# Performance work log

Hardware: AMD Instinct MI355X
Metric: run time of the kernel (lower is better)

The kernel has to match this reference:

```python
import jax, jax.numpy as jnp
import numpy as np

N_NODES = 20000
N_EDGES = 50000
IN_DIM = 128
HID = 128
OUT_DIM = 64
N_PAIRS = 128
N_LAYERS = 2
N_HEADS = 4


def setup_inputs() -> dict:
    key = jax.random.key(0)
    ks = jax.random.split(key, 32)
    s = 0.05
    def p(k, shape):
        return jax.random.normal(k, shape, jnp.float32) * s
    inp = {}
    inp["node_features"] = jax.random.normal(ks[0], (N_NODES, IN_DIM), jnp.float32)
    inp["edge_index"] = jax.random.randint(ks[1], (2, N_EDGES), 0, N_NODES, jnp.int32)
    inp["edge_timestamps"] = jax.random.uniform(ks[2], (N_EDGES,), jnp.float32)
    inp["target_pairs"] = jax.random.randint(ks[3], (N_PAIRS, 2), 0, N_NODES, jnp.int32)
    inp["in_W"] = p(ks[4], (HID, IN_DIM)); inp["in_b"] = p(ks[5], (HID,))
    inp["te_W1"] = p(ks[6], (N_LAYERS, HID, 1)); inp["te_b1"] = p(ks[7], (N_LAYERS, HID))
    inp["te_W2"] = p(ks[8], (N_LAYERS, HID, HID)); inp["te_b2"] = p(ks[9], (N_LAYERS, HID))
    inp["attn_in_W"] = p(ks[10], (N_LAYERS, 3 * HID, HID)); inp["attn_in_b"] = p(ks[11], (N_LAYERS, 3 * HID))
    inp["attn_out_W"] = p(ks[12], (N_LAYERS, HID, HID)); inp["attn_out_b"] = p(ks[13], (N_LAYERS, HID))
    inp["ft_W"] = p(ks[14], (N_LAYERS, HID, HID)); inp["ft_b"] = p(ks[15], (N_LAYERS, HID))
    inp["op_W"] = p(ks[16], (N_LAYERS, HID, HID)); inp["op_b"] = p(ks[17], (N_LAYERS, HID))
    inp["out1_W"] = p(ks[18], (HID, HID)); inp["out1_b"] = p(ks[19], (HID,))
    inp["out2_W"] = p(ks[20], (OUT_DIM, HID)); inp["out2_b"] = p(ks[21], (OUT_DIM,))
    inp["lp1_W"] = p(ks[22], (HID, 2 * OUT_DIM)); inp["lp1_b"] = p(ks[23], (HID,))
    inp["lp2_W"] = p(ks[24], (HID // 2, HID)); inp["lp2_b"] = p(ks[25], (HID // 2,))
    inp["lp3_W"] = p(ks[26], (1, HID // 2)); inp["lp3_b"] = p(ks[27], (1,))
    return inp


def _forward(node_features, edge_index, edge_timestamps, target_pairs,
             in_W, in_b, te_W1, te_b1, te_W2, te_b2,
             attn_in_W, attn_in_b, attn_out_W, attn_out_b,
             ft_W, ft_b, op_W, op_b,
             out1_W, out1_b, out2_W, out2_b,
             lp1_W, lp1_b, lp2_W, lp2_b, lp3_W, lp3_b):
    N = node_features.shape[0]
    h = in_W.shape[0]
    H = N_HEADS
    d = h // H
    scale = 1.0 / np.sqrt(d).astype(np.float32)
    src, dst = edge_index[0], edge_index[1]
    # flattened target nodes; duplicates compute identical rows so dedup (torch.unique) is unneeded
    targets = target_pairs.reshape(-1)  # [U]
    U = targets.shape[0]
    E = src.shape[0]

    x = node_features @ in_W.T + in_b  # [N, h]
    for l in range(te_W1.shape[0]):
        tf = x @ ft_W[l].T + ft_b[l]                                           # [N, h]
        tfeat = jax.nn.relu(edge_timestamps[:, None] @ te_W1[l].T + te_b1[l])
        tfeat = tfeat @ te_W2[l].T + te_b2[l]                                  # [E, h]
        Wq, Wk, Wv = jnp.split(attn_in_W[l], 3, axis=0)
        bq, bk, bv = jnp.split(attn_in_b[l], 3)
        q = (tf[targets] @ Wq.T + bq).reshape(U, H, d)
        # keys/values are linear in (tf[nbr] + tfeat): split into node term A and edge term B
        Ak = (tf @ Wk.T).reshape(N, H, d)
        Bk = (tfeat @ Wk.T + bk).reshape(E, H, d)
        Av = (tf @ Wv.T).reshape(N, H, d)
        Bv = (tfeat @ Wv.T + bv).reshape(E, H, d)
        is_src = src[None, :] == targets[:, None]          # [U, E]
        mask = is_src | (dst[None, :] == targets[:, None])  # edge incident to target
        nbr = jnp.where(is_src, dst[None, :], src[None, :])  # other endpoint, [U, E]
        qAk = jnp.einsum('uhd,nhd->uhn', q, Ak) * scale      # [U, H, N]
        idx = jnp.broadcast_to(nbr[:, None, :], (U, H, E))
        s_node = jnp.take_along_axis(qAk, idx, axis=2)        # [U, H, E]
        s_edge = jnp.einsum('uhd,ehd->uhe', q, Bk) * scale
        scores = jnp.where(mask[:, None, :], s_node + s_edge, -1e30)
        p = jax.nn.softmax(scores, axis=-1)
        p = jnp.where(mask[:, None, :], p, 0.0)               # [U, H, E]
        out_edge = jnp.einsum('uhe,ehd->uhd', p, Bv)
        # sum_e p * Av[nbr] via per-target scatter of probs into node space
        w = jax.vmap(lambda pe, ne: jax.ops.segment_sum(pe, ne, num_segments=N))(
            p.transpose(0, 2, 1), nbr)                        # [U, N, H]
        out_node = jnp.einsum('unh,nhd->uhd', w, Av)
        attn = (out_node + out_edge).reshape(U, h) @ attn_out_W[l].T + attn_out_b[l]
        has_nbr = mask.any(axis=1)
        agg_in = jnp.where(has_nbr[:, None], attn, tf[targets])
        agg = agg_in @ op_W[l].T + op_b[l]
        x = x.at[targets].set(agg)
        x = jax.nn.relu(x)
    emb = jax.nn.relu(x @ out1_W.T + out1_b) @ out2_W.T + out2_b  # [N, out]
    pair = jnp.concatenate([emb[target_pairs[:, 0]], emb[target_pairs[:, 1]]], axis=1)
    z = jax.nn.relu(pair @ lp1_W.T + lp1_b)
    z = jax.nn.relu(z @ lp2_W.T + lp2_b)
    return jax.nn.sigmoid(z @ lp3_W.T + lp3_b)  # [B, 1]


def reference(node_features, edge_index, edge_timestamps, target_pairs,
              in_W, in_b, te_W1, te_b1, te_W2, te_b2,
              attn_in_W, attn_in_b, attn_out_W, attn_out_b,
              ft_W, ft_b, op_W, op_b,
              out1_W, out1_b, out2_W, out2_b,
              lp1_W, lp1_b, lp2_W, lp2_b, lp3_W, lp3_b):
    return _forward(node_features, edge_index, edge_timestamps, target_pairs,
                    in_W, in_b, te_W1, te_b1, te_W2, te_b2,
                    attn_in_W, attn_in_b, attn_out_W, attn_out_b,
                    ft_W, ft_b, op_W, op_b,
                    out1_W, out1_b, out2_W, out2_b,
                    lp1_W, lp1_b, lp2_W, lp2_b, lp3_W, lp3_b)
```

## Files before the change

kernel.cpp:

```cpp
#include <hip/hip_runtime.h>
#include <math.h>

#define N_NODES 20000
#define N_EDGES 50000
#define N_SLOTS 256
#define N_PAIRS 128
#define CAP 32
#define MSTRIDE 16384
#define NMAT 19
#define TFLAG (1 << 30)
#define HSZ 1024
#define NBLK 256
#define BATCH 16

__device__ __forceinline__ float4 relu4(float4 v) {
    return make_float4(fmaxf(v.x, 0.f), fmaxf(v.y, 0.f), fmaxf(v.z, 0.f), fmaxf(v.w, 0.f));
}
__device__ __forceinline__ float4 add4(float4 a, float4 b) {
    return make_float4(a.x + b.x, a.y + b.y, a.z + b.z, a.w + b.w);
}
__device__ __forceinline__ void fma4(float4& acc, const float4 w, const float s) {
    acc.x = fmaf(w.x, s, acc.x); acc.y = fmaf(w.y, s, acc.y);
    acc.z = fmaf(w.z, s, acc.z); acc.w = fmaf(w.w, s, acc.w);
}
#define F4Z make_float4(0.f, 0.f, 0.f, 0.f)

__device__ __forceinline__ void gbar(unsigned* cnt, unsigned target, bool wait) {
    __syncthreads();
    if (threadIdx.x == 0) {
        __builtin_amdgcn_fence(__ATOMIC_RELEASE, "agent");
        __hip_atomic_fetch_add(cnt, 1u, __ATOMIC_RELAXED, __HIP_MEMORY_SCOPE_AGENT);
        if (wait) {
            int it = 0;
            while (true) {
                unsigned v;
                if ((it++ & 7) != 7)
                    v = __hip_atomic_load(cnt, __ATOMIC_RELAXED,
                                          __HIP_MEMORY_SCOPE_SYSTEM);
                else
                    v = __hip_atomic_fetch_add(cnt, 0u, __ATOMIC_RELAXED,
                                               __HIP_MEMORY_SCOPE_AGENT);
                if (v >= target) break;
                __builtin_amdgcn_s_sleep(16);
            }
            __builtin_amdgcn_fence(__ATOMIC_ACQUIRE, "agent");
        }
    }
    __syncthreads();
}

__device__ __forceinline__ float4 mv_ks1_g8(const float* __restrict__ WT,
                                            const float* __restrict__ xv128,
                                            int g, int jj) {
    const float4* W4 = (const float4*)WT;
    const float4* x4 = (const float4*)xv128;
    float4 acc = F4Z;
#pragma unroll
    for (int kk4 = 0; kk4 < 4; ++kk4) {
        int k4 = g * 4 + kk4;
        float4 xv = x4[k4];
        fma4(acc, W4[(k4 * 4 + 0) * 32 + jj], xv.x);
        fma4(acc, W4[(k4 * 4 + 1) * 32 + jj], xv.y);
        fma4(acc, W4[(k4 * 4 + 2) * 32 + jj], xv.z);
        fma4(acc, W4[(k4 * 4 + 3) * 32 + jj], xv.w);
    }
    return acc;
}
__device__ __forceinline__ float4 mv_ks1_g8_64(const float* __restrict__ WT,
                                               const float* __restrict__ xv128,
                                               int g, int jj) {
    const float4* W4 = (const float4*)WT;
    const float4* x4 = (const float4*)xv128;
    int j16 = jj & 15;
    float4 acc = F4Z;
#pragma unroll
    for (int kk4 = 0; kk4 < 4; ++kk4) {
        int k4 = g * 4 + kk4;
        float4 xv = x4[k4];
        fma4(acc, W4[(k4 * 4 + 0) * 16 + j16], xv.x);
        fma4(acc, W4[(k4 * 4 + 1) * 16 + j16], xv.y);
        fma4(acc, W4[(k4 * 4 + 2) * 16 + j16], xv.z);
        fma4(acc, W4[(k4 * 4 + 3) * 16 + j16], xv.w);
    }
    return acc;
}
__device__ __forceinline__ float4 comb1_g8(const float4* pb, int jj) {
    float4 s = pb[jj];
#pragma unroll
    for (int gp = 1; gp < 8; ++gp) s = add4(s, pb[gp * 32 + jj]);
    return s;
}

__device__ __forceinline__ void mv16_g8(const float* __restrict__ WT,
                                        const float* __restrict__ xs,
                                        int g, int jj, float4* acc) {
    const float4* W4 = (const float4*)WT;
    const float4* x4 = (const float4*)xs;
#pragma unroll
    for (int kk4 = 0; kk4 < 4; ++kk4) {
        int k4 = g * 4 + kk4;
        float4 w0 = W4[(k4 * 4 + 0) * 32 + jj];
        float4 w1 = W4[(k4 * 4 + 1) * 32 + jj];
        float4 w2 = W4[(k4 * 4 + 2) * 32 + jj];
        float4 w3 = W4[(k4 * 4 + 3) * 32 + jj];
#pragma unroll
        for (int e = 0; e < 16; ++e) {
            float4 xv = x4[e * 32 + k4];
            fma4(acc[e], w0, xv.x); fma4(acc[e], w1, xv.y);
            fma4(acc[e], w2, xv.z); fma4(acc[e], w3, xv.w);
        }
    }
}
__device__ __forceinline__ float4 comb16_g8(const float4* pb, int it, int jj) {
    float4 s = pb[it * 32 + jj];
#pragma unroll
    for (int gp = 1; gp < 8; ++gp) s = add4(s, pb[(gp * 16 + it) * 32 + jj]);
    return s;
}

__device__ __forceinline__ float4 mv_ks1(const float* __restrict__ WT,
                                         const float* __restrict__ xv128,
                                         int g, int jj) {
    const float4* W4 = (const float4*)WT;
    const float4* x4 = (const float4*)xv128;
    float4 acc = F4Z;
#pragma unroll 2
    for (int kk4 = 0; kk4 < 8; ++kk4) {
        int k4 = g * 8 + kk4;
        float4 xv = x4[k4];
        fma4(acc, W4[(k4 * 4 + 0) * 32 + jj], xv.x);
        fma4(acc, W4[(k4 * 4 + 1) * 32 + jj], xv.y);
        fma4(acc, W4[(k4 * 4 + 2) * 32 + jj], xv.z);
        fma4(acc, W4[(k4 * 4 + 3) * 32 + jj], xv.w);
    }
    return acc;
}
__device__ __forceinline__ float4 mv_ks1_64(const float* __restrict__ WT,
                                            const float* __restrict__ xv128,
                                            int g, int jj) {
    const float4* W4 = (const float4*)WT;
    const float4* x4 = (const float4*)xv128;
    int j16 = jj & 15;
    float4 acc = F4Z;
#pragma unroll 2
    for (int kk4 = 0; kk4 < 8; ++kk4) {
        int k4 = g * 8 + kk4;
        float4 xv = x4[k4];
        fma4(acc, W4[(k4 * 4 + 0) * 16 + j16], xv.x);
        fma4(acc, W4[(k4 * 4 + 1) * 16 + j16], xv.y);
        fma4(acc, W4[(k4 * 4 + 2) * 16 + j16], xv.z);
        fma4(acc, W4[(k4 * 4 + 3) * 16 + j16], xv.w);
    }
    return acc;
}
__device__ __forceinline__ float4 comb1(const float4* pb, int jj) {
    return add4(add4(pb[jj], pb[32 + jj]), add4(pb[64 + jj], pb[96 + jj]));
}

__device__ __forceinline__ unsigned thash(int key) {
    return ((unsigned)key * 2654435761u) >> 22;
}
__device__ __forceinline__ bool hexists(const int* __restrict__ hkey, int key) {
    unsigned h = thash(key);
    while (true) {
        int k = hkey[h];
        if (k == -1) return false;
        if (k == key) return true;
        h = (h + 1) & (HSZ - 1);
    }
}
__device__ __forceinline__ void hemit_g(const int* __restrict__ hkey,
                                        const int* __restrict__ hval,
                                        int* __restrict__ gcnt,
                                        int2* __restrict__ lst,
                                        int key, int e, int nbrf) {
    unsigned h = thash(key);
    while (true) {
        int k = hkey[h];
        if (k == -1) return;
        if (k == key) {
            int s = hval[h];
            int pos = atomicAdd(&gcnt[s], 1);
            if (pos < CAP) lst[s * CAP + pos] = make_int2(e, nbrf);
        }
        h = (h + 1) & (HSZ - 1);
    }
}

struct Params {
    const float* nf; const int* ei; const float* ts; const int* tp;
    const float* inW; const float* inb;
    const float* teW1; const float* teb1; const float* teW2; const float* teb2;
    const float* aiW; const float* aib; const float* aoW; const float* aob;
    const float* ftW; const float* ftb; const float* opW; const float* opb;
    const float* o1W; const float* o1b; const float* o2W; const float* o2b;
    const float* l1W; const float* l1b; const float* l2W; const float* l2b;
    const float* l3W; const float* l3b;
    float* out; float* x; int* cnt; int2* lst; float* emb; float* WT;
    unsigned* bar;
};

__global__ __launch_bounds__(256, 1) void k_fused(Params P) {
    __shared__ __align__(16) float xu[128], x0u[128], tfv[128], qv[128], sv[128];
    __shared__ __align__(16) float xs[BATCH * 128], t1s[BATCH * 128];
    __shared__ __align__(16) float x0s[BATCH * 128];
    __shared__ __align__(16) float zs[CAP * 128];
    __shared__ __align__(16) float4 pb[8 * 16 * 32];
    __shared__ __align__(16) float qkh[4 * 128];
    __shared__ __align__(16) float zbl[4 * 128];
    __shared__ float scl[CAP * 4], ps[CAP * 4], sbk[4];
    __shared__ int nbr_s[BATCH], tf_s[BATCH];
    __shared__ float ts_s[BATCH];
    __shared__ __align__(16) float tile[32][129];
    __shared__ int hkey[HSZ], hval[HSZ];

    const int b = blockIdx.x, tid = threadIdx.x, g = tid >> 5, jj = tid & 31;

    if (b < 72) {
        int m, r0, rows;
        if (b < 68) { m = b >> 2; r0 = (b & 3) * 32; rows = 128; }
        else { int mm = b - 68; m = 17 + (mm >> 1); r0 = (mm & 1) * 32; rows = 64; }
        const float* src;
        if (m == 0) src = P.inW;
        else if (m <= 2) src = P.ftW + (m - 1) * MSTRIDE;
        else if (m <= 4) src = P.teW2 + (m - 3) * MSTRIDE;
        else if (m <= 10) src = P.aiW + (m - 5) * MSTRIDE;
        else if (m <= 12) src = P.aoW + (m - 11) * MSTRIDE;
        else if (m <= 14) src = P.opW + (m - 13) * MSTRIDE;
        else if (m == 15) src = P.o1W;
        else if (m == 16) src = P.l1W;
        else if (m == 17) src = P.o2W;
        else src = P.l2W;
        float* dst = P.WT + m * MSTRIDE;
        for (int idx = tid; idx < 32 * 128; idx += 256) {
            int r = idx >> 7, cc = idx & 127;
            tile[r][cc] = src[(r0 + r) * 128 + cc];
        }
        __syncthreads();
        for (int idx = tid; idx < 128 * 32; idx += 256) {
            int k = idx >> 5, jr = idx & 31;
            dst[k * rows + r0 + jr] = tile[jr][k];
        }
    } else {
        for (int i = tid; i < HSZ; i += 256) hkey[i] = -1;
        __syncthreads();
        {
            int uu = P.tp[tid];
            unsigned h = thash(uu);
            while (atomicCAS(&hkey[h], -1, uu) != -1) h = (h + 1) & (HSZ - 1);
            hval[h] = tid;
        }
        __syncthreads();
        const int4* s4 = (const int4*)P.ei;
        const int4* d4 = (const int4*)(P.ei + N_EDGES);
        const int NE4 = N_EDGES / 4;
        const int nscan = NBLK - 72;
        const int chunk = (NE4 + nscan - 1) / nscan;
        const int start = (b - 72) * chunk;
        const int end = min(start + chunk, NE4);
        for (int e4 = start + tid; e4 < end; e4 += 256) {
            int4 s = s4[e4];
            int4 d = d4[e4];
            int ss[4] = {s.x, s.y, s.z, s.w};
            int dd[4] = {d.x, d.y, d.z, d.w};
#pragma unroll
            for (int t = 0; t < 4; ++t) {
                int a = ss[t], bb = dd[t];
                bool atgt = hexists(hkey, a);
                bool btgt = (bb == a) ? atgt : hexists(hkey, bb);
                if (!atgt && !btgt) continue;
                int e = e4 * 4 + t;
                if (atgt) hemit_g(hkey, hval, P.cnt, P.lst, a, e, bb | (btgt ? TFLAG : 0));
                if (btgt && bb != a) hemit_g(hkey, hval, P.cnt, P.lst, bb, e, a | (atgt ? TFLAG : 0));
            }
        }
    }
    gbar(P.bar, NBLK, true);

    const float scale = 0.17677669529663687f;
    const int u = P.tp[b];
    const int c = min(P.cnt[b], CAP);

    for (int layer = 0; layer < 2; ++layer) {
        const float* WT_in = P.WT;
        const float* WT_ft = P.WT + (1 + layer) * MSTRIDE;
        const float* WT_te2 = P.WT + (3 + layer) * MSTRIDE;
        const float* WT_q = P.WT + (5 + 3 * layer) * MSTRIDE;
        const float* WT_v = P.WT + (7 + 3 * layer) * MSTRIDE;
        const float* WT_ao = P.WT + (11 + layer) * MSTRIDE;
        const float* WT_op = P.WT + (13 + layer) * MSTRIDE;
        const float* inb = P.inb;
        const float* ftb = P.ftb + layer * 128;
        const float* teW1 = P.teW1 + layer * 128;
        const float* teb1 = P.teb1 + layer * 128;
        const float* teb2 = P.teb2 + layer * 128;
        const float* bq = P.aib + layer * 384;
        const float* bk = bq + 128;
        const float* bv = bq + 256;
        const float* aob = P.aob + layer * 128;
        const float* opb = P.opb + layer * 128;

        if (tid < 128) xu[tid] = (layer == 0) ? P.nf[(size_t)u * 128 + tid]
                                              : P.x[(size_t)u * 128 + tid];
        __syncthreads();
        const float* xeff = xu;
        if (layer == 0) {
            pb[g * 32 + jj] = mv_ks1_g8(WT_in, xu, g, jj);
            __syncthreads();
            if (g == 0)
                *(float4*)(x0u + jj * 4) = add4(comb1_g8(pb, jj), *(const float4*)(inb + jj * 4));
            xeff = x0u;
            __syncthreads();
        }
        pb[g * 32 + jj] = mv_ks1_g8(WT_ft, xeff, g, jj);
        __syncthreads();
        if (g == 0)
            *(float4*)(tfv + jj * 4) = add4(comb1_g8(pb, jj), *(const float4*)(ftb + jj * 4));
        __syncthreads();
        pb[g * 32 + jj] = mv_ks1_g8(WT_q, tfv, g, jj);
        __syncthreads();
        if (g == 0)
            *(float4*)(qv + jj * 4) = add4(comb1_g8(pb, jj), *(const float4*)(bq + jj * 4));
        __syncthreads();
        {
            const float* WkRaw = P.aiW + (size_t)layer * 3 * MSTRIDE + MSTRIDE;
            int i = tid & 127, hb = tid >> 7;
#pragma unroll
            for (int s = 0; s < 2; ++s) {
                int h = hb * 2 + s;
                float a = 0.f;
#pragma unroll 8
                for (int j = 0; j < 32; ++j)
                    a = fmaf(WkRaw[(size_t)(h * 32 + j) * 128 + i], qv[h * 32 + j], a);
                qkh[h * 128 + i] = a;
            }
            if (tid < 128) {
                float pp = qv[tid] * bk[tid];
                pp += __shfl_xor(pp, 1, 32); pp += __shfl_xor(pp, 2, 32);
                pp += __shfl_xor(pp, 4, 32); pp += __shfl_xor(pp, 8, 32);
                pp += __shfl_xor(pp, 16, 32);
                if ((tid & 31) == 0) sbk[tid >> 5] = pp;
            }
        }
        __syncthreads();

        for (int base = 0; base < c; base += BATCH) {
            if (tid < BATCH) {
                int i = base + tid;
                int2 en = (i < c) ? P.lst[b * CAP + i] : make_int2(0, 0);
                nbr_s[tid] = en.y & ~TFLAG;
                tf_s[tid] = (en.y & TFLAG) ? 1 : 0;
                ts_s[tid] = (i < c) ? P.ts[en.x] : 0.f;
            }
            __syncthreads();
            {
                int c0 = jj * 4;
                float4 w = *(const float4*)(teW1 + c0);
                float4 bb = *(const float4*)(teb1 + c0);
#pragma unroll
                for (int s = 0; s < 2; ++s) {
                    int e = g + s * 8;
                    const float* srcp = (layer == 0) ? (P.nf + (size_t)nbr_s[e] * 128 + c0)
                                                     : (P.x + (size_t)nbr_s[e] * 128 + c0);
                    float4 v = *(const float4*)srcp;
                    float* dstp = (layer == 0) ? xs : x0s;
                    *(float4*)(dstp + e * 128 + c0) = v;
                    float tse = ts_s[e];
                    *(float4*)(t1s + e * 128 + c0) =
                        make_float4(fmaxf(fmaf(tse, w.x, bb.x), 0.f),
                                    fmaxf(fmaf(tse, w.y, bb.y), 0.f),
                                    fmaxf(fmaf(tse, w.z, bb.z), 0.f),
                                    fmaxf(fmaf(tse, w.w, bb.w), 0.f));
                }
            }
            __syncthreads();
            if (layer == 0) {
                float4 acc[16] = {F4Z, F4Z, F4Z, F4Z, F4Z, F4Z, F4Z, F4Z,
                                  F4Z, F4Z, F4Z, F4Z, F4Z, F4Z, F4Z, F4Z};
                mv16_g8(WT_in, xs, g, jj, acc);
#pragma unroll
                for (int e = 0; e < 16; ++e) pb[(g * 16 + e) * 32 + jj] = acc[e];
                __syncthreads();
#pragma unroll
                for (int s = 0; s < 2; ++s) {
                    int it = 2 * g + s;
                    float4 x0v = add4(comb16_g8(pb, it, jj), *(const float4*)(inb + jj * 4));
                    *(float4*)(x0s + it * 128 + jj * 4) = x0v;
                    if (base + it < c && !tf_s[it])
                        *(float4*)(P.x + (size_t)nbr_s[it] * 128 + jj * 4) = relu4(x0v);
                }
                __syncthreads();
            }
            {
                float4 acc[16] = {F4Z, F4Z, F4Z, F4Z, F4Z, F4Z, F4Z, F4Z,
                                  F4Z, F4Z, F4Z, F4Z, F4Z, F4Z, F4Z, F4Z};
                mv16_g8(WT_ft, x0s, g, jj, acc);
                mv16_g8(WT_te2, t1s, g, jj, acc);
#pragma unroll
                for (int e = 0; e < 16; ++e) pb[(g * 16 + e) * 32 + jj] = acc[e];
                __syncthreads();
                float4 zb4 = add4(*(const float4*)(ftb + jj * 4),
                                  *(const float4*)(teb2 + jj * 4));
#pragma unroll
                for (int s = 0; s < 2; ++s) {
                    int it = 2 * g + s;
                    *(float4*)(zs + (size_t)(base + it) * 128 + jj * 4) =
                        add4(comb16_g8(pb, it, jj), zb4);
                }
                __syncthreads();
            }
            {
                int it = tid >> 4, l = tid & 15, item = base + it;
                const float* zp = zs + (size_t)item * 128;
                float s0 = 0.f, s1 = 0.f, s2 = 0.f, s3 = 0.f;
#pragma unroll
                for (int dd = 0; dd < 8; ++dd) {
                    int d = dd * 16 + l;
                    float zv = zp[d];
                    s0 = fmaf(qkh[d], zv, s0);
                    s1 = fmaf(qkh[128 + d], zv, s1);
                    s2 = fmaf(qkh[256 + d], zv, s2);
                    s3 = fmaf(qkh[384 + d], zv, s3);
                }
                s0 += __shfl_xor(s0, 1, 16); s0 += __shfl_xor(s0, 2, 16);
                s0 += __shfl_xor(s0, 4, 16); s0 += __shfl_xor(s0, 8, 16);
                s1 += __shfl_xor(s1, 1, 16); s1 += __shfl_xor(s1, 2, 16);
                s1 += __shfl_xor(s1, 4, 16); s1 += __shfl_xor(s1, 8, 16);
                s2 += __shfl_xor(s2, 1, 16); s2 += __shfl_xor(s2, 2, 16);
                s2 += __shfl_xor(s2, 4, 16); s2 += __shfl_xor(s2, 8, 16);
                s3 += __shfl_xor(s3, 1, 16); s3 += __shfl_xor(s3, 2, 16);
                s3 += __shfl_xor(s3, 4, 16); s3 += __shfl_xor(s3, 8, 16);
                if (l == 0 && item < c) {
                    scl[item * 4 + 0] = (s0 + sbk[0]) * scale;
                    scl[item * 4 + 1] = (s1 + sbk[1]) * scale;
                    scl[item * 4 + 2] = (s2 + sbk[2]) * scale;
                    scl[item * 4 + 3] = (s3 + sbk[3]) * scale;
                }
                __syncthreads();
            }
        }

        if (tid < 128 && c > 0) {
            int hd = tid >> 5, e = tid & 31;
            float m = -INFINITY;
            for (int i = 0; i < c; ++i) m = fmaxf(m, scl[i * 4 + hd]);
            float l = 0.f;
            for (int i = 0; i < c; ++i) l += __expf(scl[i * 4 + hd] - m);
            if (e < c) ps[e * 4 + hd] = __expf(scl[e * 4 + hd] - m) / l;
        }
        __syncthreads();
        {
            int i = tid & 127, hb = tid >> 7;
#pragma unroll
            for (int s = 0; s < 2; ++s) {
                int h = hb * 2 + s;
                float a = 0.f;
                for (int e = 0; e < c; ++e)
                    a = fmaf(ps[e * 4 + h], zs[(size_t)e * 128 + i], a);
                zbl[h * 128 + i] = a;
            }
        }
        __syncthreads();
        pb[g * 32 + jj] = mv_ks1_g8(WT_v, zbl + (jj >> 3) * 128, g, jj);
        __syncthreads();
        if (g == 0) {
            float4 vv = add4(comb1_g8(pb, jj), *(const float4*)(bv + jj * 4));
            if (c == 0) vv = F4Z;
            *(float4*)(sv + jj * 4) = vv;
        }
        __syncthreads();
        pb[g * 32 + jj] = mv_ks1_g8(WT_ao, sv, g, jj);
        __syncthreads();
        if (g == 0) {
            float4 z4;
            if (c > 0) z4 = add4(comb1_g8(pb, jj), *(const float4*)(aob + jj * 4));
            else z4 = *(const float4*)(tfv + jj * 4);
            *(float4*)(xu + jj * 4) = z4;
        }
        __syncthreads();
        pb[g * 32 + jj] = mv_ks1_g8(WT_op, xu, g, jj);
        __syncthreads();
        if (layer == 0) {
            if (g == 0) {
                float4 a = relu4(add4(comb1_g8(pb, jj), *(const float4*)(opb + jj * 4)));
                *(float4*)(P.x + (size_t)u * 128 + jj * 4) = a;
            }
        } else {
            if (g == 0)
                *(float4*)(x0u + jj * 4) =
                    relu4(add4(comb1_g8(pb, jj), *(const float4*)(opb + jj * 4)));
            __syncthreads();
            pb[g * 32 + jj] = mv_ks1_g8(P.WT + 15 * MSTRIDE, x0u, g, jj);
            __syncthreads();
            if (g == 0)
                *(float4*)(tfv + jj * 4) =
                    relu4(add4(comb1_g8(pb, jj), *(const float4*)(P.o1b + jj * 4)));
            __syncthreads();
            pb[g * 32 + jj] = mv_ks1_g8_64(P.WT + 17 * MSTRIDE, tfv, g, jj);
            __syncthreads();
            if (g == 0 && jj < 16)
                *(float4*)(P.emb + (size_t)b * 64 + jj * 4) =
                    add4(comb1_g8(pb, jj), *(const float4*)(P.o2b + jj * 4));
        }
        gbar(P.bar, NBLK * (2 + layer), layer == 0 || b < N_PAIRS);
    }

    if (b < N_PAIRS) {
        const float* WT_l1 = P.WT + 16 * MSTRIDE;
        const float* WT_l2 = P.WT + 18 * MSTRIDE;
        if (tid < 128)
            xu[tid] = (tid < 64) ? P.emb[(size_t)(2 * b) * 64 + tid]
                                 : P.emb[(size_t)(2 * b + 1) * 64 + (tid - 64)];
        __syncthreads();
        if (tid < 128) pb[g * 32 + jj] = mv_ks1(WT_l1, xu, g, jj);
        __syncthreads();
        if (tid < 128 && g == 0)
            *(float4*)(tfv + jj * 4) =
                relu4(add4(comb1(pb, jj), *(const float4*)(P.l1b + jj * 4)));
        __syncthreads();
        if (tid < 128) pb[g * 32 + jj] = mv_ks1_64(WT_l2, tfv, g, jj);
        __syncthreads();
        if (tid < 128 && g == 0 && jj < 16)
            *(float4*)(qv + jj * 4) =
                relu4(add4(comb1(pb, jj), *(const float4*)(P.l2b + jj * 4)));
        __syncthreads();
        if (tid < 64) {
            float v = qv[tid] * P.l3W[tid];
            v += __shfl_xor(v, 1);
            v += __shfl_xor(v, 2);
            v += __shfl_xor(v, 4);
            v += __shfl_xor(v, 8);
            v += __shfl_xor(v, 16);
            v += __shfl_xor(v, 32);
            if (tid == 0) P.out[b] = 1.f / (1.f + __expf(-(v + P.l3b[0])));
        }
    }
}

extern "C" void kernel_launch(void* const* d_in, const int* in_sizes, int n_in,
                              void* d_out, int out_size, void* d_ws, size_t ws_size,
                              hipStream_t stream) {
    Params P;
    P.nf  = (const float*)d_in[0];
    P.ei  = (const int*)d_in[1];
    P.ts  = (const float*)d_in[2];
    P.tp  = (const int*)d_in[3];
    P.inW = (const float*)d_in[4];
    P.inb = (const float*)d_in[5];
    P.teW1 = (const float*)d_in[6];
    P.teb1 = (const float*)d_in[7];
    P.teW2 = (const float*)d_in[8];
    P.teb2 = (const float*)d_in[9];
    P.aiW = (const float*)d_in[10];
    P.aib = (const float*)d_in[11];
    P.aoW = (const float*)d_in[12];
    P.aob = (const float*)d_in[13];
    P.ftW = (const float*)d_in[14];
    P.ftb = (const float*)d_in[15];
    P.opW = (const float*)d_in[16];
    P.opb = (const float*)d_in[17];
    P.o1W = (const float*)d_in[18];
    P.o1b = (const float*)d_in[19];
    P.o2W = (const float*)d_in[20];
    P.o2b = (const float*)d_in[21];
    P.l1W = (const float*)d_in[22];
    P.l1b = (const float*)d_in[23];
    P.l2W = (const float*)d_in[24];
    P.l2b = (const float*)d_in[25];
    P.l3W = (const float*)d_in[26];
    P.l3b = (const float*)d_in[27];
    P.out = (float*)d_out;

    char* ws = (char*)d_ws;
    size_t off = 0;
    P.x    = (float*)(ws + off); off += (size_t)N_NODES * 128 * 4;
    P.cnt  = (int*)  (ws + off); off += N_SLOTS * 4;
    P.lst  = (int2*) (ws + off); off += (size_t)N_SLOTS * CAP * 8;
    P.emb  = (float*)(ws + off); off += N_SLOTS * 64 * 4;
    P.WT   = (float*)(ws + off); off += (size_t)NMAT * MSTRIDE * 4;
    P.bar  = (unsigned*)(ws + off); off += 256;

    hipMemsetAsync(P.cnt, 0, N_SLOTS * 4, stream);
    hipMemsetAsync(P.bar, 0, 4, stream);
    k_fused<<<NBLK, 256, 0, stream>>>(P);
}
```

Baseline: 196.2 us.

## Replace final grid barrier with per-pair flags and load node features into registers

Drops the last grid-wide barrier after layer 1. Each block now sets a per-slot ready flag once its embedding is written, and each link-prediction block waits only on the two flags it needs. Node feature rows are loaded straight into registers for the first matvec, which skips a shared-memory staging step and one __syncthreads. The barrier spin sleep is also shortened to react faster, at the cost of more polling traffic.

```diff
diff --git a/kernel.cpp b/kernel.cpp
--- a/kernel.cpp
+++ b/kernel.cpp
@@ -41,7 +41,7 @@
                     v = __hip_atomic_fetch_add(cnt, 0u, __ATOMIC_RELAXED,
                                                __HIP_MEMORY_SCOPE_AGENT);
                 if (v >= target) break;
-                __builtin_amdgcn_s_sleep(16);
+                __builtin_amdgcn_s_sleep(8);
             }
             __builtin_amdgcn_fence(__ATOMIC_ACQUIRE, "agent");
         }
@@ -63,6 +63,21 @@
         fma4(acc, W4[(k4 * 4 + 1) * 32 + jj], xv.y);
         fma4(acc, W4[(k4 * 4 + 2) * 32 + jj], xv.z);
         fma4(acc, W4[(k4 * 4 + 3) * 32 + jj], xv.w);
+    }
+    return acc;
+}
+__device__ __forceinline__ float4 mv_reg_g8(const float* __restrict__ WT,
+                                            const float4 xv[4], int g, int jj) {
+    const float4* W4 = (const float4*)WT;
+    float4 acc = F4Z;
+#pragma unroll
+    for (int kk4 = 0; kk4 < 4; ++kk4) {
+        int k4 = g * 4 + kk4;
+        float4 x = xv[kk4];
+        fma4(acc, W4[(k4 * 4 + 0) * 32 + jj], x.x);
+        fma4(acc, W4[(k4 * 4 + 1) * 32 + jj], x.y);
+        fma4(acc, W4[(k4 * 4 + 2) * 32 + jj], x.z);
+        fma4(acc, W4[(k4 * 4 + 3) * 32 + jj], x.w);
     }
     return acc;
 }
@@ -197,7 +212,7 @@
     const float* l1W; const float* l1b; const float* l2W; const float* l2b;
     const float* l3W; const float* l3b;
     float* out; float* x; int* cnt; int2* lst; float* emb; float* WT;
-    unsigned* bar;
+    unsigned* bar; unsigned* flg;
 };
 
 __global__ __launch_bounds__(256, 1) void k_fused(Params P) {
@@ -300,19 +315,25 @@
         const float* aob = P.aob + layer * 128;
         const float* opb = P.opb + layer * 128;
 
-        if (tid < 128) xu[tid] = (layer == 0) ? P.nf[(size_t)u * 128 + tid]
-                                              : P.x[(size_t)u * 128 + tid];
-        __syncthreads();
-        const float* xeff = xu;
-        if (layer == 0) {
-            pb[g * 32 + jj] = mv_ks1_g8(WT_in, xu, g, jj);
-            __syncthreads();
-            if (g == 0)
-                *(float4*)(x0u + jj * 4) = add4(comb1_g8(pb, jj), *(const float4*)(inb + jj * 4));
-            xeff = x0u;
-            __syncthreads();
-        }
-        pb[g * 32 + jj] = mv_ks1_g8(WT_ft, xeff, g, jj);
+        {
+            const float* xsrc = (layer == 0) ? (P.nf + (size_t)u * 128)
+                                             : (P.x + (size_t)u * 128);
+            float4 xva[4];
+#pragma unroll
+            for (int cc = 0; cc < 4; ++cc)
+                xva[cc] = *(const float4*)(xsrc + (g * 4 + cc) * 4);
+            if (layer == 0) {
+                pb[g * 32 + jj] = mv_reg_g8(WT_in, xva, g, jj);
+                __syncthreads();
+                if (g == 0)
+                    *(float4*)(x0u + jj * 4) =
+                        add4(comb1_g8(pb, jj), *(const float4*)(inb + jj * 4));
+                __syncthreads();
+                pb[g * 32 + jj] = mv_ks1_g8(WT_ft, x0u, g, jj);
+            } else {
+                pb[g * 32 + jj] = mv_reg_g8(WT_ft, xva, g, jj);
+            }
+        }
         __syncthreads();
         if (g == 0)
             *(float4*)(tfv + jj * 4) = add4(comb1_g8(pb, jj), *(const float4*)(ftb + jj * 4));
@@ -485,6 +506,7 @@
                 float4 a = relu4(add4(comb1_g8(pb, jj), *(const float4*)(opb + jj * 4)));
                 *(float4*)(P.x + (size_t)u * 128 + jj * 4) = a;
             }
+            gbar(P.bar, NBLK * 2, true);
         } else {
             if (g == 0)
                 *(float4*)(x0u + jj * 4) =
@@ -501,11 +523,25 @@
             if (g == 0 && jj < 16)
                 *(float4*)(P.emb + (size_t)b * 64 + jj * 4) =
                     add4(comb1_g8(pb, jj), *(const float4*)(P.o2b + jj * 4));
-        }
-        gbar(P.bar, NBLK * (2 + layer), layer == 0 || b < N_PAIRS);
+            __syncthreads();
+            if (tid == 0) {
+                __builtin_amdgcn_fence(__ATOMIC_RELEASE, "agent");
+                __hip_atomic_store(&P.flg[b], 1u, __ATOMIC_RELAXED,
+                                   __HIP_MEMORY_SCOPE_AGENT);
+            }
+        }
     }
 
     if (b < N_PAIRS) {
+        if (tid == 0) {
+            while (__hip_atomic_load(&P.flg[2 * b], __ATOMIC_RELAXED,
+                                     __HIP_MEMORY_SCOPE_SYSTEM) == 0u ||
+                   __hip_atomic_load(&P.flg[2 * b + 1], __ATOMIC_RELAXED,
+                                     __HIP_MEMORY_SCOPE_SYSTEM) == 0u)
+                __builtin_amdgcn_s_sleep(4);
+            __builtin_amdgcn_fence(__ATOMIC_ACQUIRE, "agent");
+        }
+        __syncthreads();
         const float* WT_l1 = P.WT + 16 * MSTRIDE;
         const float* WT_l2 = P.WT + 18 * MSTRIDE;
         if (tid < 128)
@@ -578,9 +614,10 @@
     P.lst  = (int2*) (ws + off); off += (size_t)N_SLOTS * CAP * 8;
     P.emb  = (float*)(ws + off); off += N_SLOTS * 64 * 4;
     P.WT   = (float*)(ws + off); off += (size_t)NMAT * MSTRIDE * 4;
-    P.bar  = (unsigned*)(ws + off); off += 256;
+    P.bar  = (unsigned*)(ws + off); off += 4;
+    P.flg  = (unsigned*)(ws + off); off += N_SLOTS * 4;
 
     hipMemsetAsync(P.cnt, 0, N_SLOTS * 4, stream);
-    hipMemsetAsync(P.bar, 0, 4, stream);
+    hipMemsetAsync(P.bar, 0, 4 + N_SLOTS * 4, stream);
     k_fused<<<NBLK, 256, 0, stream>>>(P);
 }
```

Measured after the change: 226.3 us. +15.3%, slower.
